# Kernel optimization log

Hardware: AMD Instinct MI355X
Metric: run time of the kernel (lower is better)

The kernel has to match this reference:

```python
import jax, jax.numpy as jnp
import numpy as np

N, E, D_IN, D_HID, D_OUT = 50000, 800000, 128, 128, 300
BN_EPS = 1e-5


def setup_inputs() -> dict:
    key = jax.random.key(0)
    ks = jax.random.split(key, 10)
    s_in = 1.0 / np.sqrt(D_IN)
    s_hid = 1.0 / np.sqrt(D_HID)
    return {
        "x": jax.random.normal(ks[0], (N, D_IN), jnp.float32),
        "edge_index": jax.random.randint(ks[1], (2, E), 0, N, jnp.int64),
        "Wl": jax.random.normal(ks[2], (D_IN, D_HID), jnp.float32) * s_in,
        "bl": jnp.zeros((D_HID,), jnp.float32),
        "Wr": jax.random.normal(ks[3], (D_IN, D_HID), jnp.float32) * s_in,
        "Wsk": jax.random.normal(ks[4], (D_IN, D_HID), jnp.float32) * s_in,
        "bsk": jnp.zeros((D_HID,), jnp.float32),
        "gamma": jnp.ones((D_HID,), jnp.float32),
        "beta": jnp.zeros((D_HID,), jnp.float32),
        "rmean": jnp.zeros((D_HID,), jnp.float32),
        "rvar": jnp.ones((D_HID,), jnp.float32),
        "Wlo": jax.random.normal(ks[5], (D_HID, D_OUT), jnp.float32) * s_hid,
        "blo": jnp.zeros((D_OUT,), jnp.float32),
        "Wro": jax.random.normal(ks[6], (D_HID, D_OUT), jnp.float32) * s_hid,
    }


def sage_conv(x, src, dst, n_nodes, W_l, b_l, W_r):
    # PyG SAGEConv (aggr='mean'): lin_l(mean_{j in N(i)} x_j) + lin_r(x_i)
    msgs = x[src]                                                 # [E, d] gather
    agg = jax.ops.segment_sum(msgs, dst, num_segments=n_nodes)    # [N, d]
    cnt = jax.ops.segment_sum(jnp.ones((src.shape[0], 1), x.dtype), dst,
                              num_segments=n_nodes)               # [N, 1]
    mean = agg / jnp.maximum(cnt, 1.0)
    return mean @ W_l + b_l + x @ W_r


def reference(x, edge_index, Wl, bl, Wr, Wsk, bsk, gamma, beta, rmean, rvar,
              Wlo, blo, Wro):
    src, dst = edge_index[0], edge_index[1]
    n = x.shape[0]
    # layer 0: conv + skip linear
    h = sage_conv(x, src, dst, n, Wl, bl, Wr) + (x @ Wsk + bsk)
    # BatchNorm1d (eval: running stats)
    h = (h - rmean) * (gamma * jax.lax.rsqrt(rvar + BN_EPS)) + beta
    x_emb = jax.nn.relu(h)                                        # dropout: no-op in eval
    # output conv + log_softmax
    x_out = sage_conv(x_emb, src, dst, n, Wlo, blo, Wro)
    return h, jax.nn.log_softmax(x_out, axis=1)
```

## Files before the change

kernel.cpp:

```cpp
#include <hip/hip_runtime.h>

typedef __attribute__((__ext_vector_type__(8))) __bf16 bf16x8;
typedef __attribute__((__ext_vector_type__(4))) float f32x4;
typedef __attribute__((__ext_vector_type__(2))) float f32x2;
typedef __attribute__((__ext_vector_type__(4))) unsigned int u32x4;

__device__ __forceinline__ float bf2f(unsigned short u) {
    return __uint_as_float(((unsigned int)u) << 16);
}
__device__ __forceinline__ unsigned short f2bf(float f) {
    unsigned int u = __float_as_uint(f);
    u += 0x7FFFu + ((u >> 16) & 1u);
    return (unsigned short)(u >> 16);
}

__device__ __forceinline__ bool low_short_is_bf16like(unsigned int w) {
    unsigned int lo = w & 0xFFFFu;
    if (lo == 0u || lo == 0x8000u) return true;
    unsigned int e = (lo >> 7) & 0xFFu;
    return (e >= 0x6Cu && e <= 0x8Cu);
}
__device__ __forceinline__ int probe_f32(const unsigned int* __restrict__ p) {
    int t = threadIdx.x & 63;
    int cnt = __popcll(__ballot(low_short_is_bf16like(p[t])));
    return (cnt < 32) ? 1 : 0;
}
__device__ __forceinline__ int probe_e64(const unsigned int* __restrict__ ei) {
    int t = threadIdx.x & 63;
    unsigned int o1 = ei[2 * t + 1];
    unsigned int o2 = ei[2 * t + 129];
    return __all((o1 == 0u) && (o2 == 0u)) ? 1 : 0;
}

__global__ __launch_bounds__(256) void k_tobf(
    const void* __restrict__ xv, unsigned short* __restrict__ xbf,
    unsigned int* __restrict__ x8, int* __restrict__ deg,
    long nelem, int n, int tgrid)
{
    if ((int)blockIdx.x >= tgrid) {
        int j = ((int)blockIdx.x - tgrid) * 256 + threadIdx.x;
        if (j < n) deg[j] = 0;
        return;
    }
    int xf32 = probe_f32((const unsigned int*)xv);
    long i = ((long)blockIdx.x * 256 + threadIdx.x) * 8;
    if (i >= nelem) return;
    float f[8];
    if (xf32) {
        const float4* p = (const float4*)((const float*)xv + i);
        float4 v0 = p[0], v1 = p[1];
        f[0] = v0.x; f[1] = v0.y; f[2] = v0.z; f[3] = v0.w;
        f[4] = v1.x; f[5] = v1.y; f[6] = v1.z; f[7] = v1.w;
        u32x4 o;
        o.x = (unsigned int)f2bf(f[0]) | ((unsigned int)f2bf(f[1]) << 16);
        o.y = (unsigned int)f2bf(f[2]) | ((unsigned int)f2bf(f[3]) << 16);
        o.z = (unsigned int)f2bf(f[4]) | ((unsigned int)f2bf(f[5]) << 16);
        o.w = (unsigned int)f2bf(f[6]) | ((unsigned int)f2bf(f[7]) << 16);
        *(u32x4*)&xbf[i] = o;
    } else {
        u32x4 v = *(const u32x4*)((const unsigned short*)xv + i);
        *(u32x4*)&xbf[i] = v;
        f[0] = bf2f((unsigned short)v.x); f[1] = bf2f((unsigned short)(v.x >> 16));
        f[2] = bf2f((unsigned short)v.y); f[3] = bf2f((unsigned short)(v.y >> 16));
        f[4] = bf2f((unsigned short)v.z); f[5] = bf2f((unsigned short)(v.z >> 16));
        f[6] = bf2f((unsigned short)v.w); f[7] = bf2f((unsigned short)(v.w >> 16));
    }
    unsigned int q0 = 0, q1 = 0;
    q0 = (unsigned int)__builtin_amdgcn_cvt_pk_fp8_f32(f[0], f[1], (int)q0, false);
    q0 = (unsigned int)__builtin_amdgcn_cvt_pk_fp8_f32(f[2], f[3], (int)q0, true);
    q1 = (unsigned int)__builtin_amdgcn_cvt_pk_fp8_f32(f[4], f[5], (int)q1, false);
    q1 = (unsigned int)__builtin_amdgcn_cvt_pk_fp8_f32(f[6], f[7], (int)q1, true);
    uint2 q; q.x = q0; q.y = q1;
    *(uint2*)&x8[i >> 2] = q;
}

__global__ __launch_bounds__(256) void k_fold(
    const void* __restrict__ Wl, const void* __restrict__ Wr,
    const void* __restrict__ Wsk, const void* __restrict__ gamma,
    const void* __restrict__ rvar, const void* __restrict__ bl,
    const void* __restrict__ bsk, const void* __restrict__ rmean,
    const void* __restrict__ beta, const void* __restrict__ Wlo,
    const void* __restrict__ blo, const void* __restrict__ Wro,
    unsigned short* __restrict__ W1p, unsigned short* __restrict__ W2p,
    float* __restrict__ bias1, float* __restrict__ bias2)
{
    int wf32 = probe_f32((const unsigned int*)Wl);
    int b = blockIdx.x, t = threadIdx.x;
    if (b < 128) {
        int idx = b * 256 + t;
        int kb = idx >> 10, c = (idx >> 3) & 127, k7 = idx & 7;
        int k = kb * 8 + k7;
        float g, rv, w;
        if (wf32) {
            g  = ((const float*)gamma)[c];
            rv = ((const float*)rvar)[c];
            if (k < 128) w = ((const float*)Wl)[k * 128 + c];
            else { int kk = k - 128;
                   w = ((const float*)Wr)[kk * 128 + c] + ((const float*)Wsk)[kk * 128 + c]; }
        } else {
            g  = bf2f(((const unsigned short*)gamma)[c]);
            rv = bf2f(((const unsigned short*)rvar)[c]);
            if (k < 128) w = bf2f(((const unsigned short*)Wl)[k * 128 + c]);
            else { int kk = k - 128;
                   w = bf2f(((const unsigned short*)Wr)[kk * 128 + c]) +
                       bf2f(((const unsigned short*)Wsk)[kk * 128 + c]); }
        }
        float s = g * rsqrtf(rv + 1e-5f);
        W1p[idx] = f2bf(w * s);
    } else if (b < 448) {
        int idx = (b - 128) * 256 + t;
        int kb = idx / 2560;
        int rem = idx - kb * 2560;
        int c = rem >> 3, k7 = idx & 7;
        int k = kb * 8 + k7;
        float w = 0.f;
        if (c < 300) {
            if (wf32)
                w = (k < 128) ? ((const float*)Wlo)[k * 300 + c]
                              : ((const float*)Wro)[(k - 128) * 300 + c];
            else
                w = (k < 128) ? bf2f(((const unsigned short*)Wlo)[k * 300 + c])
                              : bf2f(((const unsigned short*)Wro)[(k - 128) * 300 + c]);
        }
        W2p[idx] = f2bf(w);
    } else {
        if (t < 128) {
            float g, rv, b1, b2, rm, be;
            if (wf32) {
                g = ((const float*)gamma)[t]; rv = ((const float*)rvar)[t];
                b1 = ((const float*)bl)[t];   b2 = ((const float*)bsk)[t];
                rm = ((const float*)rmean)[t]; be = ((const float*)beta)[t];
            } else {
                g = bf2f(((const unsigned short*)gamma)[t]); rv = bf2f(((const unsigned short*)rvar)[t]);
                b1 = bf2f(((const unsigned short*)bl)[t]);   b2 = bf2f(((const unsigned short*)bsk)[t]);
                rm = bf2f(((const unsigned short*)rmean)[t]); be = bf2f(((const unsigned short*)beta)[t]);
            }
            float s = g * rsqrtf(rv + 1e-5f);
            bias1[t] = (b1 + b2 - rm) * s + be;
        }
        for (int c = t; c < 320; c += 256) {
            float v = 0.f;
            if (c < 300)
                v = wf32 ? ((const float*)blo)[c] : bf2f(((const unsigned short*)blo)[c]);
            bias2[c] = v;
        }
    }
}

__global__ __launch_bounds__(256) void k_rank(
    const int* __restrict__ ei,
    int* __restrict__ deg, int* __restrict__ rank,
    unsigned int* __restrict__ ds32, int E, int nnodes, int pack)
{
    int e64 = probe_e64((const unsigned int*)ei);
    int e = blockIdx.x * 256 + threadIdx.x;
    if (e >= E) return;
    int s, d;
    if (e64) { s = ei[2 * e]; d = ei[2 * (E + e)]; }
    else     { s = ei[e];     d = ei[E + e]; }
    if ((unsigned)s >= (unsigned)nnodes) s = 0;
    int r = 0;
    if ((unsigned)d < (unsigned)nnodes) r = atomicAdd(&deg[d], 1);
    rank[e] = r;
    if (pack) ds32[e] = (((unsigned int)d & 0xFFFFu) << 16) | ((unsigned int)s & 0xFFFFu);
}

__global__ __launch_bounds__(256) void k_place16(
    const unsigned int* __restrict__ ds32,
    const int* __restrict__ rowptr, const int* __restrict__ aux,
    const int* __restrict__ rank,
    unsigned short* __restrict__ adj, int E, int nnodes)
{
    int e = blockIdx.x * 256 + threadIdx.x;
    if (e >= E) return;
    unsigned int ds = ds32[e];
    int d = (int)(ds >> 16);
    unsigned short s = (unsigned short)(ds & 0xFFFFu);
    if (d >= nnodes) return;
    adj[rowptr[d] + aux[d >> 10] + rank[e]] = s;
}

__global__ __launch_bounds__(256) void k_place32(
    const int* __restrict__ ei,
    const int* __restrict__ rowptr, const int* __restrict__ aux,
    const int* __restrict__ rank,
    int* __restrict__ adj, int E, int nnodes)
{
    int e64 = probe_e64((const unsigned int*)ei);
    int e = blockIdx.x * 256 + threadIdx.x;
    if (e >= E) return;
    int s, d;
    if (e64) { s = ei[2 * e]; d = ei[2 * (E + e)]; }
    else     { s = ei[e];     d = ei[E + e]; }
    if ((unsigned)d >= (unsigned)nnodes) return;
    if ((unsigned)s >= (unsigned)nnodes) s = 0;
    adj[rowptr[d] + aux[d >> 10] + rank[e]] = s;
}

__global__ __launch_bounds__(256) void k_scan_a(
    const int* __restrict__ deg, int* __restrict__ rowptr,
    int* __restrict__ aux, int n)
{
    __shared__ int wsum[4];
    int t = threadIdx.x, blk = blockIdx.x;
    int base = blk * 1024 + t * 4;
    int v[4];
    int s = 0;
    #pragma unroll
    for (int i = 0; i < 4; i++) { int idx = base + i; v[i] = (idx < n) ? deg[idx] : 0; s += v[i]; }
    int lane = t & 63, wv = t >> 6;
    int inc = s;
    #pragma unroll
    for (int off = 1; off < 64; off <<= 1) {
        int u = __shfl_up(inc, off);
        if (lane >= off) inc += u;
    }
    if (lane == 63) wsum[wv] = inc;
    __syncthreads();
    int woff = 0;
    if (wv >= 1) woff += wsum[0];
    if (wv >= 2) woff += wsum[1];
    if (wv >= 3) woff += wsum[2];
    int exc = woff + inc - s;
    #pragma unroll
    for (int i = 0; i < 4; i++) { int idx = base + i; if (idx < n) rowptr[idx] = exc; exc += v[i]; }
    if (t == 255) aux[blk] = woff + inc;
}

__global__ __launch_bounds__(64) void k_scan_b(int* __restrict__ aux, int nblk)
{
    int t = threadIdx.x;
    int carry = 0;
    for (int base = 0; base < nblk; base += 64) {
        int idx = base + t;
        int v = (idx < nblk) ? aux[idx] : 0;
        int inc = v;
        #pragma unroll
        for (int off = 1; off < 64; off <<= 1) {
            int u = __shfl_up(inc, off);
            if (t >= off) inc += u;
        }
        if (idx < nblk) aux[idx] = carry + inc - v;
        carry += __shfl(inc, 63);
    }
}

template <typename IT>
__global__ __launch_bounds__(256) void k_agg(
    const unsigned int* __restrict__ x8,
    const int* __restrict__ rowptr, const int* __restrict__ aux,
    const int* __restrict__ deg,
    const IT* __restrict__ adj, unsigned short* __restrict__ meanB, int n)
{
    int wid = (blockIdx.x * 256 + threadIdx.x) >> 6;
    if (wid >= n) return;
    int lane = threadIdx.x & 63;
    int h  = lane >> 5;
    int sl = lane & 31;
    int start = rowptr[wid] + aux[wid >> 10];
    int dc = deg[wid];
    float acc[4][4];
    #pragma unroll
    for (int u = 0; u < 4; u++)
        #pragma unroll
        for (int c = 0; c < 4; c++) acc[u][c] = 0.f;
    int i = 0;
    for (; i + 15 < dc; i += 16) {
        int e[8]; unsigned int p[8];
        #pragma unroll
        for (int u = 0; u < 8; u++) e[u] = (int)adj[start + i + 2 * u + h];
        #pragma unroll
        for (int u = 0; u < 8; u++) p[u] = x8[(size_t)e[u] * 32 + sl];
        #pragma unroll
        for (int u = 0; u < 8; u++) {
            f32x2 lo = __builtin_amdgcn_cvt_pk_f32_fp8((int)p[u], false);
            f32x2 hi = __builtin_amdgcn_cvt_pk_f32_fp8((int)p[u], true);
            acc[u & 3][0] += lo.x; acc[u & 3][1] += lo.y;
            acc[u & 3][2] += hi.x; acc[u & 3][3] += hi.y;
        }
    }
    if (i + 7 < dc) {
        int e[4]; unsigned int p[4];
        #pragma unroll
        for (int u = 0; u < 4; u++) e[u] = (int)adj[start + i + 2 * u + h];
        #pragma unroll
        for (int u = 0; u < 4; u++) p[u] = x8[(size_t)e[u] * 32 + sl];
        #pragma unroll
        for (int u = 0; u < 4; u++) {
            f32x2 lo = __builtin_amdgcn_cvt_pk_f32_fp8((int)p[u], false);
            f32x2 hi = __builtin_amdgcn_cvt_pk_f32_fp8((int)p[u], true);
            acc[u][0] += lo.x; acc[u][1] += lo.y;
            acc[u][2] += hi.x; acc[u][3] += hi.y;
        }
        i += 8;
    }
    for (; i + h < dc; i += 2) {
        int e0 = (int)adj[start + i + h];
        unsigned int p0 = x8[(size_t)e0 * 32 + sl];
        f32x2 lo = __builtin_amdgcn_cvt_pk_f32_fp8((int)p0, false);
        f32x2 hi = __builtin_amdgcn_cvt_pk_f32_fp8((int)p0, true);
        acc[0][0] += lo.x; acc[0][1] += lo.y; acc[0][2] += hi.x; acc[0][3] += hi.y;
    }
    float t0 = (acc[0][0] + acc[1][0]) + (acc[2][0] + acc[3][0]);
    float t1 = (acc[0][1] + acc[1][1]) + (acc[2][1] + acc[3][1]);
    float t2 = (acc[0][2] + acc[1][2]) + (acc[2][2] + acc[3][2]);
    float t3 = (acc[0][3] + acc[1][3]) + (acc[2][3] + acc[3][3]);
    t0 += __shfl_xor(t0, 32);
    t1 += __shfl_xor(t1, 32);
    t2 += __shfl_xor(t2, 32);
    t3 += __shfl_xor(t3, 32);
    if (h == 0) {
        float inv = 1.f / fmaxf((float)dc, 1.f);
        uint2 o;
        o.x = (unsigned int)f2bf(t0 * inv) | ((unsigned int)f2bf(t1 * inv) << 16);
        o.y = (unsigned int)f2bf(t2 * inv) | ((unsigned int)f2bf(t3 * inv) << 16);
        *(uint2*)&meanB[(size_t)wid * 128 + sl * 4] = o;
    }
}

__global__ __launch_bounds__(256) void k_gemm1(
    const unsigned short* __restrict__ meanB,
    const unsigned short* __restrict__ xbf, const unsigned int* __restrict__ xprobe,
    const unsigned short* __restrict__ Wp,
    const float* __restrict__ bias, void* __restrict__ outh,
    unsigned short* __restrict__ xemb, unsigned int* __restrict__ xemb8, int nrows)
{
    constexpr int NTW = 2;
    __shared__ __align__(16) unsigned short Alds[32 * 264];
    int tid = threadIdx.x;
    int row0 = blockIdx.x * 32;
    int xf32 = probe_f32(xprobe);
    {
        int r = tid >> 3, c0 = (tid & 7) * 16;
        int rg = row0 + r; if (rg >= nrows) rg = nrows - 1;
        const u32x4* mp = (const u32x4*)(meanB + (size_t)rg * 128 + c0);
        *(u32x4*)&Alds[r * 264 + c0]     = mp[0];
        *(u32x4*)&Alds[r * 264 + c0 + 8] = mp[1];
        const u32x4* xp = (const u32x4*)(xbf + (size_t)rg * 128 + c0);
        *(u32x4*)&Alds[r * 264 + 128 + c0]     = xp[0];
        *(u32x4*)&Alds[r * 264 + 128 + c0 + 8] = xp[1];
    }
    __syncthreads();
    f32x4 acc[2][NTW];
    #pragma unroll
    for (int a = 0; a < 2; a++)
        #pragma unroll
        for (int b = 0; b < NTW; b++) acc[a][b] = f32x4{0.f, 0.f, 0.f, 0.f};
    int lane = tid & 63, wv = tid >> 6, lh = lane & 15, lq = lane >> 4;
    bf16x8 bcur[NTW], bnxt[NTW];
    #pragma unroll
    for (int i = 0; i < NTW; i++)
        bcur[i] = *(const bf16x8*)&Wp[lq * 1024 + ((wv + 4 * i) * 16 + lh) * 8];
    #pragma unroll
    for (int ks = 0; ks < 8; ++ks) {
        if (ks < 7) {
            #pragma unroll
            for (int i = 0; i < NTW; i++)
                bnxt[i] = *(const bf16x8*)&Wp[((ks + 1) * 4 + lq) * 1024 + ((wv + 4 * i) * 16 + lh) * 8];
        }
        bf16x8 a0 = *(const bf16x8*)&Alds[lh * 264 + ks * 32 + lq * 8];
        bf16x8 a1 = *(const bf16x8*)&Alds[(16 + lh) * 264 + ks * 32 + lq * 8];
        #pragma unroll
        for (int i = 0; i < NTW; i++) {
            acc[0][i] = __builtin_amdgcn_mfma_f32_16x16x32_bf16(a0, bcur[i], acc[0][i], 0, 0, 0);
            acc[1][i] = __builtin_amdgcn_mfma_f32_16x16x32_bf16(a1, bcur[i], acc[1][i], 0, 0, 0);
        }
        #pragma unroll
        for (int i = 0; i < NTW; i++) bcur[i] = bnxt[i];
    }
    __syncthreads();
    float* outF = (float*)outh;
    unsigned short* outB = (unsigned short*)outh;
    #pragma unroll
    for (int rt = 0; rt < 2; ++rt)
        #pragma unroll
        for (int i = 0; i < NTW; i++)
            #pragma unroll
            for (int j = 0; j < 4; j++) {
                int rl = rt * 16 + lq * 4 + j;
                int r = row0 + rl;
                int c = (wv + 4 * i) * 16 + lh;
                float v = acc[rt][i][j] + bias[c];
                float rv = fmaxf(v, 0.f);
                unsigned short rb = f2bf(rv);
                Alds[rl * 264 + c] = rb;
                if (r < nrows) {
                    if (xf32) __builtin_nontemporal_store(v, &outF[(size_t)r * 128 + c]);
                    else      outB[(size_t)r * 128 + c] = f2bf(v);
                    xemb[(size_t)r * 128 + c] = rb;
                }
            }
    __syncthreads();
    {
        int r = tid >> 3, c0 = (tid & 7) * 16;
        int rg = row0 + r;
        if (rg < nrows) {
            u32x4 va = *(u32x4*)&Alds[r * 264 + c0];
            u32x4 vb = *(u32x4*)&Alds[r * 264 + c0 + 8];
            u32x4 q;
            unsigned int w;
            w = 0;
            w = (unsigned int)__builtin_amdgcn_cvt_pk_fp8_f32(
                    bf2f((unsigned short)va.x), bf2f((unsigned short)(va.x >> 16)), (int)w, false);
            w = (unsigned int)__builtin_amdgcn_cvt_pk_fp8_f32(
                    bf2f((unsigned short)va.y), bf2f((unsigned short)(va.y >> 16)), (int)w, true);
            q.x = w;
            w = 0;
            w = (unsigned int)__builtin_amdgcn_cvt_pk_fp8_f32(
                    bf2f((unsigned short)va.z), bf2f((unsigned short)(va.z >> 16)), (int)w, false);
            w = (unsigned int)__builtin_amdgcn_cvt_pk_fp8_f32(
                    bf2f((unsigned short)va.w), bf2f((unsigned short)(va.w >> 16)), (int)w, true);
            q.y = w;
            w = 0;
            w = (unsigned int)__builtin_amdgcn_cvt_pk_fp8_f32(
                    bf2f((unsigned short)vb.x), bf2f((unsigned short)(vb.x >> 16)), (int)w, false);
            w = (unsigned int)__builtin_amdgcn_cvt_pk_fp8_f32(
                    bf2f((unsigned short)vb.y), bf2f((unsigned short)(vb.y >> 16)), (int)w, true);
            q.z = w;
            w = 0;
            w = (unsigned int)__builtin_amdgcn_cvt_pk_fp8_f32(
                    bf2f((unsigned short)vb.z), bf2f((unsigned short)(vb.z >> 16)), (int)w, false);
            w = (unsigned int)__builtin_amdgcn_cvt_pk_fp8_f32(
                    bf2f((unsigned short)vb.w), bf2f((unsigned short)(vb.w >> 16)), (int)w, true);
            q.w = w;
            *(u32x4*)&xemb8[(size_t)rg * 32 + (tid & 7) * 4] = q;
        }
    }
}

__global__ __launch_bounds__(256) void k_gemm2(
    const unsigned short* __restrict__ meanB,
    const unsigned short* __restrict__ xf, const unsigned int* __restrict__ xprobe,
    const unsigned short* __restrict__ Wp,
    const float* __restrict__ bias, void* __restrict__ outbase, int nrows)
{
    constexpr int NTW = 5;
    __shared__ __align__(16) unsigned short Alds[32 * 264];
    __shared__ float redM[4][32];
    __shared__ float redS[4][32];
    int tid = threadIdx.x;
    int row0 = blockIdx.x * 32;
    int xf32 = probe_f32(xprobe);
    {
        int r = tid >> 3, c0 = (tid & 7) * 16;
        int rg = row0 + r; if (rg >= nrows) rg = nrows - 1;
        const u32x4* mp = (const u32x4*)(meanB + (size_t)rg * 128 + c0);
        *(u32x4*)&Alds[r * 264 + c0]     = mp[0];
        *(u32x4*)&Alds[r * 264 + c0 + 8] = mp[1];
        const u32x4* xp = (const u32x4*)(xf + (size_t)rg * 128 + c0);
        *(u32x4*)&Alds[r * 264 + 128 + c0]     = xp[0];
        *(u32x4*)&Alds[r * 264 + 128 + c0 + 8] = xp[1];
    }
    __syncthreads();
    f32x4 acc[2][NTW];
    #pragma unroll
    for (int a = 0; a < 2; a++)
        #pragma unroll
        for (int b = 0; b < NTW; b++) acc[a][b] = f32x4{0.f, 0.f, 0.f, 0.f};
    int lane = tid & 63, wv = tid >> 6, lh = lane & 15, lq = lane >> 4;
    bf16x8 bcur[NTW], bnxt[NTW];
    #pragma unroll
    for (int i = 0; i < NTW; i++)
        bcur[i] = *(const bf16x8*)&Wp[lq * 2560 + ((wv + 4 * i) * 16 + lh) * 8];
    #pragma unroll
    for (int ks = 0; ks < 8; ++ks) {
        if (ks < 7) {
            #pragma unroll
            for (int i = 0; i < NTW; i++)
                bnxt[i] = *(const bf16x8*)&Wp[((ks + 1) * 4 + lq) * 2560 + ((wv + 4 * i) * 16 + lh) * 8];
        }
        bf16x8 a0 = *(const bf16x8*)&Alds[lh * 264 + ks * 32 + lq * 8];
        bf16x8 a1 = *(const bf16x8*)&Alds[(16 + lh) * 264 + ks * 32 + lq * 8];
        #pragma unroll
        for (int i = 0; i < NTW; i++) {
            acc[0][i] = __builtin_amdgcn_mfma_f32_16x16x32_bf16(a0, bcur[i], acc[0][i], 0, 0, 0);
            acc[1][i] = __builtin_amdgcn_mfma_f32_16x16x32_bf16(a1, bcur[i], acc[1][i], 0, 0, 0);
        }
        #pragma unroll
        for (int i = 0; i < NTW; i++) bcur[i] = bnxt[i];
    }
    #pragma unroll
    for (int rt = 0; rt < 2; ++rt)
        #pragma unroll
        for (int i = 0; i < NTW; i++) {
            int col = (wv + 4 * i) * 16 + lh;
            float b = bias[col];
            #pragma unroll
            for (int j = 0; j < 4; j++) acc[rt][i][j] += b;
        }
    float M[2][4];
    #pragma unroll
    for (int rt = 0; rt < 2; ++rt)
        #pragma unroll
        for (int j = 0; j < 4; j++) {
            float m = -3.0e38f;
            #pragma unroll
            for (int i = 0; i < NTW; i++) {
                int col = (wv + 4 * i) * 16 + lh;
                if (col < 300) m = fmaxf(m, acc[rt][i][j]);
            }
            m = fmaxf(m, __shfl_xor(m, 1, 16));
            m = fmaxf(m, __shfl_xor(m, 2, 16));
            m = fmaxf(m, __shfl_xor(m, 4, 16));
            m = fmaxf(m, __shfl_xor(m, 8, 16));
            M[rt][j] = m;
        }
    if (lh == 0) {
        #pragma unroll
        for (int rt = 0; rt < 2; ++rt)
            #pragma unroll
            for (int j = 0; j < 4; j++)
                redM[wv][rt * 16 + lq * 4 + j] = M[rt][j];
    }
    __syncthreads();
    #pragma unroll
    for (int rt = 0; rt < 2; ++rt)
        #pragma unroll
        for (int j = 0; j < 4; j++) {
            int rl = rt * 16 + lq * 4 + j;
            M[rt][j] = fmaxf(fmaxf(redM[0][rl], redM[1][rl]),
                             fmaxf(redM[2][rl], redM[3][rl]));
        }
    float S[2][4];
    #pragma unroll
    for (int rt = 0; rt < 2; ++rt)
        #pragma unroll
        for (int j = 0; j < 4; j++) {
            float s = 0.f;
            #pragma unroll
            for (int i = 0; i < NTW; i++) {
                int col = (wv + 4 * i) * 16 + lh;
                if (col < 300) s += __expf(acc[rt][i][j] - M[rt][j]);
            }
            s += __shfl_xor(s, 1, 16);
            s += __shfl_xor(s, 2, 16);
            s += __shfl_xor(s, 4, 16);
            s += __shfl_xor(s, 8, 16);
            S[rt][j] = s;
        }
    if (lh == 0) {
        #pragma unroll
        for (int rt = 0; rt < 2; ++rt)
            #pragma unroll
            for (int j = 0; j < 4; j++)
                redS[wv][rt * 16 + lq * 4 + j] = S[rt][j];
    }
    __syncthreads();
    float* out1F = (float*)outbase + (size_t)nrows * 128;
    unsigned short* out1B = (unsigned short*)outbase + (size_t)nrows * 128;
    #pragma unroll
    for (int rt = 0; rt < 2; ++rt)
        #pragma unroll
        for (int j = 0; j < 4; j++) {
            int rl = rt * 16 + lq * 4 + j;
            float Sall = (redS[0][rl] + redS[1][rl]) + (redS[2][rl] + redS[3][rl]);
            float L = M[rt][j] + __logf(Sall);
            int rg = row0 + rl;
            if (rg < nrows) {
                #pragma unroll
                for (int i = 0; i < NTW; i++) {
                    int col = (wv + 4 * i) * 16 + lh;
                    if (col < 300) {
                        float v = acc[rt][i][j] - L;
                        if (xf32) out1F[(size_t)rg * 300 + col] = v;
                        else      out1B[(size_t)rg * 300 + col] = f2bf(v);
                    }
                }
            }
        }
}

extern "C" void kernel_launch(void* const* d_in, const int* in_sizes, int n_in,
                              void* d_out, int out_size, void* d_ws, size_t ws_size,
                              hipStream_t stream)
{
    const void* x     = d_in[0];
    const int*  ei    = (const int*)d_in[1];
    const void* Wl    = d_in[2];
    const void* bl    = d_in[3];
    const void* Wr    = d_in[4];
    const void* Wsk   = d_in[5];
    const void* bsk   = d_in[6];
    const void* gamma = d_in[7];
    const void* beta  = d_in[8];
    const void* rmean = d_in[9];
    const void* rvar  = d_in[10];
    const void* Wlo   = d_in[11];
    const void* blo   = d_in[12];
    const void* Wro   = d_in[13];

    int N = in_sizes[0] / 128;
    int E = in_sizes[1] / 2;
    long nelem = (long)N * 128;
    bool idx16 = (N <= 65535);

    char* ws = (char*)d_ws;
    size_t off = 0;
    unsigned short* xbf   = (unsigned short*)(ws + off); off += (size_t)N * 128 * 2;
    unsigned short* meanB = (unsigned short*)(ws + off); off += (size_t)N * 128 * 2;
    unsigned short* xemb  = (unsigned short*)(ws + off); off += (size_t)N * 128 * 2;
    unsigned int* x8      = (unsigned int*)(ws + off);   off += (size_t)N * 128;
    unsigned int* xemb8   = (unsigned int*)(ws + off);   off += (size_t)N * 128;
    off = (off + 255) & ~(size_t)255;
    int* deg    = (int*)(ws + off);           off += (size_t)N * 4;
    int* rowptr = (int*)(ws + off);           off += (size_t)N * 4;
    int* rank   = (int*)(ws + off);           off += (size_t)E * 4;
    unsigned int* ds32 = (unsigned int*)(ws + off); off += (size_t)E * 4;
    int* aux    = (int*)(ws + off);           off += 256;
    void* adjv  = (void*)(ws + off);          off += (size_t)E * 4;
    off = (off + 255) & ~(size_t)255;
    unsigned short* W1p = (unsigned short*)(ws + off);  off += 32768 * 2;
    unsigned short* W2p = (unsigned short*)(ws + off);  off += 81920 * 2;
    float* bias1 = (float*)(ws + off);        off += 512;
    float* bias2 = (float*)(ws + off);        off += 1280;

    int egrid = (E + 255) / 256;
    int sblk  = (N + 1023) / 1024;
    int agrid = (N + 3) / 4;
    int ggrid = (N + 31) / 32;
    int tgrid = (int)((nelem / 8 + 255) / 256);
    int dgrid = (N + 255) / 256;

    const unsigned int* xprobe = (const unsigned int*)x;

    k_tobf<<<tgrid + dgrid, 256, 0, stream>>>(x, xbf, x8, deg, nelem, N, tgrid);
    k_fold<<<449, 256, 0, stream>>>(Wl, Wr, Wsk, gamma, rvar, bl, bsk, rmean, beta,
                                    Wlo, blo, Wro, W1p, W2p, bias1, bias2);

    k_rank<<<egrid, 256, 0, stream>>>(ei, deg, rank, ds32, E, N, idx16 ? 1 : 0);
    k_scan_a<<<sblk, 256, 0, stream>>>(deg, rowptr, aux, N);
    k_scan_b<<<1, 64, 0, stream>>>(aux, sblk);

    if (idx16) {
        unsigned short* adj = (unsigned short*)adjv;
        k_place16<<<egrid, 256, 0, stream>>>(ds32, rowptr, aux, rank, adj, E, N);
        k_agg<unsigned short><<<agrid, 256, 0, stream>>>(x8, rowptr, aux, deg, adj, meanB, N);
        k_gemm1<<<ggrid, 256, 0, stream>>>(meanB, xbf, xprobe, W1p, bias1, d_out, xemb, xemb8, N);
        k_agg<unsigned short><<<agrid, 256, 0, stream>>>(xemb8, rowptr, aux, deg, adj, meanB, N);
        k_gemm2<<<ggrid, 256, 0, stream>>>(meanB, xemb, xprobe, W2p, bias2, d_out, N);
    } else {
        int* adj = (int*)adjv;
        k_place32<<<egrid, 256, 0, stream>>>(ei, rowptr, aux, rank, adj, E, N);
        k_agg<int><<<agrid, 256, 0, stream>>>(x8, rowptr, aux, deg, adj, meanB, N);
        k_gemm1<<<ggrid, 256, 0, stream>>>(meanB, xbf, xprobe, W1p, bias1, d_out, xemb, xemb8, N);
        k_agg<int><<<agrid, 256, 0, stream>>>(xemb8, rowptr, aux, deg, adj, meanB, N);
        k_gemm2<<<ggrid, 256, 0, stream>>>(meanB, xemb, xprobe, W2p, bias2, d_out, N);
    }
}
```

Baseline: 171.3 us.

## Fuse front-end kernels and drop bf16 x_emb copy in favor of fp8

Merges the edge-rank, x conversion and weight-fold kernels into one launch, and replaces the deg zeroing with a memset. The layer-0 GEMM no longer writes a bf16 copy of x_emb. The second GEMM instead reads the fp8 copy and converts it to bf16 when staging to LDS. This cuts launches and roughly 12.8 MB of global traffic, at the cost of fp8 precision in the lin_r term of the output layer.

```diff
diff --git a/kernel.cpp b/kernel.cpp
--- a/kernel.cpp
+++ b/kernel.cpp
@@ -32,49 +32,11 @@
     return __all((o1 == 0u) && (o2 == 0u)) ? 1 : 0;
 }
 
-__global__ __launch_bounds__(256) void k_tobf(
+__global__ __launch_bounds__(256) void k_front(
+    const int* __restrict__ ei, int* __restrict__ deg, int* __restrict__ rank,
+    unsigned int* __restrict__ ds32, int E, int nnodes, int pack, int egrid,
     const void* __restrict__ xv, unsigned short* __restrict__ xbf,
-    unsigned int* __restrict__ x8, int* __restrict__ deg,
-    long nelem, int n, int tgrid)
-{
-    if ((int)blockIdx.x >= tgrid) {
-        int j = ((int)blockIdx.x - tgrid) * 256 + threadIdx.x;
-        if (j < n) deg[j] = 0;
-        return;
-    }
-    int xf32 = probe_f32((const unsigned int*)xv);
-    long i = ((long)blockIdx.x * 256 + threadIdx.x) * 8;
-    if (i >= nelem) return;
-    float f[8];
-    if (xf32) {
-        const float4* p = (const float4*)((const float*)xv + i);
-        float4 v0 = p[0], v1 = p[1];
-        f[0] = v0.x; f[1] = v0.y; f[2] = v0.z; f[3] = v0.w;
-        f[4] = v1.x; f[5] = v1.y; f[6] = v1.z; f[7] = v1.w;
-        u32x4 o;
-        o.x = (unsigned int)f2bf(f[0]) | ((unsigned int)f2bf(f[1]) << 16);
-        o.y = (unsigned int)f2bf(f[2]) | ((unsigned int)f2bf(f[3]) << 16);
-        o.z = (unsigned int)f2bf(f[4]) | ((unsigned int)f2bf(f[5]) << 16);
-        o.w = (unsigned int)f2bf(f[6]) | ((unsigned int)f2bf(f[7]) << 16);
-        *(u32x4*)&xbf[i] = o;
-    } else {
-        u32x4 v = *(const u32x4*)((const unsigned short*)xv + i);
-        *(u32x4*)&xbf[i] = v;
-        f[0] = bf2f((unsigned short)v.x); f[1] = bf2f((unsigned short)(v.x >> 16));
-        f[2] = bf2f((unsigned short)v.y); f[3] = bf2f((unsigned short)(v.y >> 16));
-        f[4] = bf2f((unsigned short)v.z); f[5] = bf2f((unsigned short)(v.z >> 16));
-        f[6] = bf2f((unsigned short)v.w); f[7] = bf2f((unsigned short)(v.w >> 16));
-    }
-    unsigned int q0 = 0, q1 = 0;
-    q0 = (unsigned int)__builtin_amdgcn_cvt_pk_fp8_f32(f[0], f[1], (int)q0, false);
-    q0 = (unsigned int)__builtin_amdgcn_cvt_pk_fp8_f32(f[2], f[3], (int)q0, true);
-    q1 = (unsigned int)__builtin_amdgcn_cvt_pk_fp8_f32(f[4], f[5], (int)q1, false);
-    q1 = (unsigned int)__builtin_amdgcn_cvt_pk_fp8_f32(f[6], f[7], (int)q1, true);
-    uint2 q; q.x = q0; q.y = q1;
-    *(uint2*)&x8[i >> 2] = q;
-}
-
-__global__ __launch_bounds__(256) void k_fold(
+    unsigned int* __restrict__ x8, long nelem, int tgrid,
     const void* __restrict__ Wl, const void* __restrict__ Wr,
     const void* __restrict__ Wsk, const void* __restrict__ gamma,
     const void* __restrict__ rvar, const void* __restrict__ bl,
@@ -84,8 +46,56 @@
     unsigned short* __restrict__ W1p, unsigned short* __restrict__ W2p,
     float* __restrict__ bias1, float* __restrict__ bias2)
 {
+    int blk = blockIdx.x, t = threadIdx.x;
+    if (blk < egrid) {
+        int e64 = probe_e64((const unsigned int*)ei);
+        int e = blk * 256 + t;
+        if (e >= E) return;
+        int s, d;
+        if (e64) { s = ei[2 * e]; d = ei[2 * (E + e)]; }
+        else     { s = ei[e];     d = ei[E + e]; }
+        if ((unsigned)s >= (unsigned)nnodes) s = 0;
+        int r = 0;
+        if ((unsigned)d < (unsigned)nnodes) r = atomicAdd(&deg[d], 1);
+        rank[e] = r;
+        if (pack) ds32[e] = (((unsigned int)d & 0xFFFFu) << 16) | ((unsigned int)s & 0xFFFFu);
+        return;
+    }
+    if (blk < egrid + tgrid) {
+        int xf32 = probe_f32((const unsigned int*)xv);
+        long i = ((long)(blk - egrid) * 256 + t) * 8;
+        if (i >= nelem) return;
+        float f[8];
+        if (xf32) {
+            const float4* p = (const float4*)((const float*)xv + i);
+            float4 v0 = p[0], v1 = p[1];
+            f[0] = v0.x; f[1] = v0.y; f[2] = v0.z; f[3] = v0.w;
+            f[4] = v1.x; f[5] = v1.y; f[6] = v1.z; f[7] = v1.w;
+            u32x4 o;
+            o.x = (unsigned int)f2bf(f[0]) | ((unsigned int)f2bf(f[1]) << 16);
+            o.y = (unsigned int)f2bf(f[2]) | ((unsigned int)f2bf(f[3]) << 16);
+            o.z = (unsigned int)f2bf(f[4]) | ((unsigned int)f2bf(f[5]) << 16);
+            o.w = (unsigned int)f2bf(f[6]) | ((unsigned int)f2bf(f[7]) << 16);
+            *(u32x4*)&xbf[i] = o;
+        } else {
+            u32x4 v = *(const u32x4*)((const unsigned short*)xv + i);
+            *(u32x4*)&xbf[i] = v;
+            f[0] = bf2f((unsigned short)v.x); f[1] = bf2f((unsigned short)(v.x >> 16));
+            f[2] = bf2f((unsigned short)v.y); f[3] = bf2f((unsigned short)(v.y >> 16));
+            f[4] = bf2f((unsigned short)v.z); f[5] = bf2f((unsigned short)(v.z >> 16));
+            f[6] = bf2f((unsigned short)v.w); f[7] = bf2f((unsigned short)(v.w >> 16));
+        }
+        unsigned int q0 = 0, q1 = 0;
+        q0 = (unsigned int)__builtin_amdgcn_cvt_pk_fp8_f32(f[0], f[1], (int)q0, false);
+        q0 = (unsigned int)__builtin_amdgcn_cvt_pk_fp8_f32(f[2], f[3], (int)q0, true);
+        q1 = (unsigned int)__builtin_amdgcn_cvt_pk_fp8_f32(f[4], f[5], (int)q1, false);
+        q1 = (unsigned int)__builtin_amdgcn_cvt_pk_fp8_f32(f[6], f[7], (int)q1, true);
+        uint2 q; q.x = q0; q.y = q1;
+        *(uint2*)&x8[i >> 2] = q;
+        return;
+    }
     int wf32 = probe_f32((const unsigned int*)Wl);
-    int b = blockIdx.x, t = threadIdx.x;
+    int b = blk - egrid - tgrid;
     if (b < 128) {
         int idx = b * 256 + t;
         int kb = idx >> 10, c = (idx >> 3) & 127, k7 = idx & 7;
@@ -147,22 +157,52 @@
     }
 }
 
-__global__ __launch_bounds__(256) void k_rank(
-    const int* __restrict__ ei,
-    int* __restrict__ deg, int* __restrict__ rank,
-    unsigned int* __restrict__ ds32, int E, int nnodes, int pack)
-{
-    int e64 = probe_e64((const unsigned int*)ei);
-    int e = blockIdx.x * 256 + threadIdx.x;
-    if (e >= E) return;
-    int s, d;
-    if (e64) { s = ei[2 * e]; d = ei[2 * (E + e)]; }
-    else     { s = ei[e];     d = ei[E + e]; }
-    if ((unsigned)s >= (unsigned)nnodes) s = 0;
-    int r = 0;
-    if ((unsigned)d < (unsigned)nnodes) r = atomicAdd(&deg[d], 1);
-    rank[e] = r;
-    if (pack) ds32[e] = (((unsigned int)d & 0xFFFFu) << 16) | ((unsigned int)s & 0xFFFFu);
+__global__ __launch_bounds__(256) void k_scan_a(
+    const int* __restrict__ deg, int* __restrict__ rowptr,
+    int* __restrict__ aux, int n)
+{
+    __shared__ int wsum[4];
+    int t = threadIdx.x, blk = blockIdx.x;
+    int base = blk * 1024 + t * 4;
+    int v[4];
+    int s = 0;
+    #pragma unroll
+    for (int i = 0; i < 4; i++) { int idx = base + i; v[i] = (idx < n) ? deg[idx] : 0; s += v[i]; }
+    int lane = t & 63, wv = t >> 6;
+    int inc = s;
+    #pragma unroll
+    for (int off = 1; off < 64; off <<= 1) {
+        int u = __shfl_up(inc, off);
+        if (lane >= off) inc += u;
+    }
+    if (lane == 63) wsum[wv] = inc;
+    __syncthreads();
+    int woff = 0;
+    if (wv >= 1) woff += wsum[0];
+    if (wv >= 2) woff += wsum[1];
+    if (wv >= 3) woff += wsum[2];
+    int exc = woff + inc - s;
+    #pragma unroll
+    for (int i = 0; i < 4; i++) { int idx = base + i; if (idx < n) rowptr[idx] = exc; exc += v[i]; }
+    if (t == 255) aux[blk] = woff + inc;
+}
+
+__global__ __launch_bounds__(64) void k_scan_b(int* __restrict__ aux, int nblk)
+{
+    int t = threadIdx.x;
+    int carry = 0;
+    for (int base = 0; base < nblk; base += 64) {
+        int idx = base + t;
+        int v = (idx < nblk) ? aux[idx] : 0;
+        int inc = v;
+        #pragma unroll
+        for (int off = 1; off < 64; off <<= 1) {
+            int u = __shfl_up(inc, off);
+            if (t >= off) inc += u;
+        }
+        if (idx < nblk) aux[idx] = carry + inc - v;
+        carry += __shfl(inc, 63);
+    }
 }
 
 __global__ __launch_bounds__(256) void k_place16(
@@ -195,54 +235,6 @@
     if ((unsigned)d >= (unsigned)nnodes) return;
     if ((unsigned)s >= (unsigned)nnodes) s = 0;
     adj[rowptr[d] + aux[d >> 10] + rank[e]] = s;
-}
-
-__global__ __launch_bounds__(256) void k_scan_a(
-    const int* __restrict__ deg, int* __restrict__ rowptr,
-    int* __restrict__ aux, int n)
-{
-    __shared__ int wsum[4];
-    int t = threadIdx.x, blk = blockIdx.x;
-    int base = blk * 1024 + t * 4;
-    int v[4];
-    int s = 0;
-    #pragma unroll
-    for (int i = 0; i < 4; i++) { int idx = base + i; v[i] = (idx < n) ? deg[idx] : 0; s += v[i]; }
-    int lane = t & 63, wv = t >> 6;
-    int inc = s;
-    #pragma unroll
-    for (int off = 1; off < 64; off <<= 1) {
-        int u = __shfl_up(inc, off);
-        if (lane >= off) inc += u;
-    }
-    if (lane == 63) wsum[wv] = inc;
-    __syncthreads();
-    int woff = 0;
-    if (wv >= 1) woff += wsum[0];
-    if (wv >= 2) woff += wsum[1];
-    if (wv >= 3) woff += wsum[2];
-    int exc = woff + inc - s;
-    #pragma unroll
-    for (int i = 0; i < 4; i++) { int idx = base + i; if (idx < n) rowptr[idx] = exc; exc += v[i]; }
-    if (t == 255) aux[blk] = woff + inc;
-}
-
-__global__ __launch_bounds__(64) void k_scan_b(int* __restrict__ aux, int nblk)
-{
-    int t = threadIdx.x;
-    int carry = 0;
-    for (int base = 0; base < nblk; base += 64) {
-        int idx = base + t;
-        int v = (idx < nblk) ? aux[idx] : 0;
-        int inc = v;
-        #pragma unroll
-        for (int off = 1; off < 64; off <<= 1) {
-            int u = __shfl_up(inc, off);
-            if (t >= off) inc += u;
-        }
-        if (idx < nblk) aux[idx] = carry + inc - v;
-        carry += __shfl(inc, 63);
-    }
 }
 
 template <typename IT>
@@ -323,7 +315,7 @@
     const unsigned short* __restrict__ xbf, const unsigned int* __restrict__ xprobe,
     const unsigned short* __restrict__ Wp,
     const float* __restrict__ bias, void* __restrict__ outh,
-    unsigned short* __restrict__ xemb, unsigned int* __restrict__ xemb8, int nrows)
+    unsigned int* __restrict__ xemb8, int nrows)
 {
     constexpr int NTW = 2;
     __shared__ __align__(16) unsigned short Alds[32 * 264];
@@ -381,13 +373,10 @@
                 int r = row0 + rl;
                 int c = (wv + 4 * i) * 16 + lh;
                 float v = acc[rt][i][j] + bias[c];
-                float rv = fmaxf(v, 0.f);
-                unsigned short rb = f2bf(rv);
-                Alds[rl * 264 + c] = rb;
+                Alds[rl * 264 + c] = f2bf(fmaxf(v, 0.f));
                 if (r < nrows) {
                     if (xf32) __builtin_nontemporal_store(v, &outF[(size_t)r * 128 + c]);
                     else      outB[(size_t)r * 128 + c] = f2bf(v);
-                    xemb[(size_t)r * 128 + c] = rb;
                 }
             }
     __syncthreads();
@@ -430,7 +419,7 @@
 
 __global__ __launch_bounds__(256) void k_gemm2(
     const unsigned short* __restrict__ meanB,
-    const unsigned short* __restrict__ xf, const unsigned int* __restrict__ xprobe,
+    const unsigned int* __restrict__ xemb8, const unsigned int* __restrict__ xprobe,
     const unsigned short* __restrict__ Wp,
     const float* __restrict__ bias, void* __restrict__ outbase, int nrows)
 {
@@ -447,9 +436,17 @@
         const u32x4* mp = (const u32x4*)(meanB + (size_t)rg * 128 + c0);
         *(u32x4*)&Alds[r * 264 + c0]     = mp[0];
         *(u32x4*)&Alds[r * 264 + c0 + 8] = mp[1];
-        const u32x4* xp = (const u32x4*)(xf + (size_t)rg * 128 + c0);
-        *(u32x4*)&Alds[r * 264 + 128 + c0]     = xp[0];
-        *(u32x4*)&Alds[r * 264 + 128 + c0 + 8] = xp[1];
+        u32x4 q = *(const u32x4*)&xemb8[(size_t)rg * 32 + (c0 >> 2)];
+        #pragma unroll
+        for (int k = 0; k < 4; k++) {
+            unsigned int w = (k == 0) ? q.x : (k == 1) ? q.y : (k == 2) ? q.z : q.w;
+            f32x2 lo = __builtin_amdgcn_cvt_pk_f32_fp8((int)w, false);
+            f32x2 hi = __builtin_amdgcn_cvt_pk_f32_fp8((int)w, true);
+            unsigned int p0 = (unsigned int)f2bf(lo.x) | ((unsigned int)f2bf(lo.y) << 16);
+            unsigned int p1 = (unsigned int)f2bf(hi.x) | ((unsigned int)f2bf(hi.y) << 16);
+            *(unsigned int*)&Alds[r * 264 + 128 + c0 + k * 4]     = p0;
+            *(unsigned int*)&Alds[r * 264 + 128 + c0 + k * 4 + 2] = p1;
+        }
     }
     __syncthreads();
     f32x4 acc[2][NTW];
@@ -598,7 +595,6 @@
     size_t off = 0;
     unsigned short* xbf   = (unsigned short*)(ws + off); off += (size_t)N * 128 * 2;
     unsigned short* meanB = (unsigned short*)(ws + off); off += (size_t)N * 128 * 2;
-    unsigned short* xemb  = (unsigned short*)(ws + off); off += (size_t)N * 128 * 2;
     unsigned int* x8      = (unsigned int*)(ws + off);   off += (size_t)N * 128;
     unsigned int* xemb8   = (unsigned int*)(ws + off);   off += (size_t)N * 128;
     off = (off + 255) & ~(size_t)255;
@@ -619,15 +615,17 @@
     int agrid = (N + 3) / 4;
     int ggrid = (N + 31) / 32;
     int tgrid = (int)((nelem / 8 + 255) / 256);
-    int dgrid = (N + 255) / 256;
 
     const unsigned int* xprobe = (const unsigned int*)x;
 
-    k_tobf<<<tgrid + dgrid, 256, 0, stream>>>(x, xbf, x8, deg, nelem, N, tgrid);
-    k_fold<<<449, 256, 0, stream>>>(Wl, Wr, Wsk, gamma, rvar, bl, bsk, rmean, beta,
-                                    Wlo, blo, Wro, W1p, W2p, bias1, bias2);
-
-    k_rank<<<egrid, 256, 0, stream>>>(ei, deg, rank, ds32, E, N, idx16 ? 1 : 0);
+    hipMemsetAsync(deg, 0, (size_t)N * 4, stream);
+
+    k_front<<<egrid + tgrid + 449, 256, 0, stream>>>(
+        ei, deg, rank, ds32, E, N, idx16 ? 1 : 0, egrid,
+        x, xbf, x8, nelem, tgrid,
+        Wl, Wr, Wsk, gamma, rvar, bl, bsk, rmean, beta, Wlo, blo, Wro,
+        W1p, W2p, bias1, bias2);
+
     k_scan_a<<<sblk, 256, 0, stream>>>(deg, rowptr, aux, N);
     k_scan_b<<<1, 64, 0, stream>>>(aux, sblk);
 
@@ -635,15 +633,15 @@
         unsigned short* adj = (unsigned short*)adjv;
         k_place16<<<egrid, 256, 0, stream>>>(ds32, rowptr, aux, rank, adj, E, N);
         k_agg<unsigned short><<<agrid, 256, 0, stream>>>(x8, rowptr, aux, deg, adj, meanB, N);
-        k_gemm1<<<ggrid, 256, 0, stream>>>(meanB, xbf, xprobe, W1p, bias1, d_out, xemb, xemb8, N);
+        k_gemm1<<<ggrid, 256, 0, stream>>>(meanB, xbf, xprobe, W1p, bias1, d_out, xemb8, N);
         k_agg<unsigned short><<<agrid, 256, 0, stream>>>(xemb8, rowptr, aux, deg, adj, meanB, N);
-        k_gemm2<<<ggrid, 256, 0, stream>>>(meanB, xemb, xprobe, W2p, bias2, d_out, N);
+        k_gemm2<<<ggrid, 256, 0, stream>>>(meanB, xemb8, xprobe, W2p, bias2, d_out, N);
     } else {
         int* adj = (int*)adjv;
         k_place32<<<egrid, 256, 0, stream>>>(ei, rowptr, aux, rank, adj, E, N);
         k_agg<int><<<agrid, 256, 0, stream>>>(x8, rowptr, aux, deg, adj, meanB, N);
-        k_gemm1<<<ggrid, 256, 0, stream>>>(meanB, xbf, xprobe, W1p, bias1, d_out, xemb, xemb8, N);
+        k_gemm1<<<ggrid, 256, 0, stream>>>(meanB, xbf, xprobe, W1p, bias1, d_out, xemb8, N);
         k_agg<int><<<agrid, 256, 0, stream>>>(xemb8, rowptr, aux, deg, adj, meanB, N);
-        k_gemm2<<<ggrid, 256, 0, stream>>>(meanB, xemb, xprobe, W2p, bias2, d_out, N);
-    }
-}
+        k_gemm2<<<ggrid, 256, 0, stream>>>(meanB, xemb8, xprobe, W2p, bias2, d_out, N);
+    }
+}
```

New measurement: 168.1 us. Within noise of the previous version (-1.9%).
